# Kernel tuning notes

Measured on AMD Instinct MI355X. Metric: run time of the kernel, lower is better.

The kernel has to match this reference:

```python
import jax, jax.numpy as jnp
import numpy as np

B, LQ, LKV = 4, 2048, 2048
E, AUG, H = 2048, 1024, 16
DH = E // H
EPS = 1e-6


def setup_inputs() -> dict:
    key = jax.random.key(0)
    ks = jax.random.split(key, 6)
    s = lambda d: 1.0 / np.sqrt(d)
    return {
        "query": jax.random.normal(ks[0], (B, LQ, E), jnp.float32),
        "aug_hidden_state": jax.random.normal(ks[1], (B, LKV, AUG), jnp.float32),
        "aug_mask": jnp.ones((B, LKV), jnp.float32),
        "proj_w": jax.random.normal(ks[2], (E, AUG), jnp.float32) * s(AUG),
        "proj_b": jnp.zeros((E,), jnp.float32),
        "in_proj_w": jax.random.normal(ks[3], (3 * E, E), jnp.float32) * s(E),
        "in_proj_b": jnp.zeros((3 * E,), jnp.float32),
        "out_proj_w": jax.random.normal(ks[4], (E, E), jnp.float32) * s(E),
        "out_proj_b": jnp.zeros((E,), jnp.float32),
        "rms_w": jnp.zeros((E,), jnp.float32),
    }


def reference(query, aug_hidden_state, aug_mask, proj_w, proj_b,
              in_proj_w, in_proj_b, out_proj_w, out_proj_b, rms_w):
    del aug_mask  # asserted but never used by the original forward
    # key and value: two identical Linear calls in the original -> same tensor
    kv = aug_hidden_state @ proj_w.T + proj_b                      # [B,LKV,E]
    wq, wk, wv = jnp.split(in_proj_w, 3, axis=0)
    bq, bk, bv = jnp.split(in_proj_b, 3, axis=0)
    q = (query @ wq.T + bq).reshape(B, LQ, H, DH)
    k = (kv @ wk.T + bk).reshape(B, LKV, H, DH)
    v = (kv @ wv.T + bv).reshape(B, LKV, H, DH)
    scale = 1.0 / np.sqrt(DH)
    scores = jnp.einsum("bqhd,bkhd->bhqk", q * scale, k)           # [B,H,LQ,LKV]
    attn = jax.nn.softmax(scores, axis=-1)
    ctx = jnp.einsum("bhqk,bkhd->bqhd", attn, v).reshape(B, LQ, E)
    attn_out = ctx @ out_proj_w.T + out_proj_b                      # [B,LQ,E]
    # GemmaRMSNorm: fp32 norm, (1 + weight) gain
    x32 = attn_out.astype(jnp.float32)
    normed = x32 * jax.lax.rsqrt(jnp.mean(x32 * x32, axis=-1, keepdims=True) + EPS)
    attn_out = (normed * (1.0 + rms_w)).astype(attn_out.dtype)
    return attn_out + query
```

## Files before the change

kernel.cpp:

```cpp
#include <hip/hip_runtime.h>
#include <hip/hip_bf16.h>
#include <stdint.h>

#define B_   4
#define LQ_  2048
#define LKV_ 2048
#define E_   2048
#define AUG_ 1024
#define H_   16
#define DH_  128

typedef unsigned short u16;
typedef __bf16 bf16x8 __attribute__((ext_vector_type(8)));
typedef float f32x4 __attribute__((ext_vector_type(4)));
typedef float f32x16 __attribute__((ext_vector_type(16)));
typedef int i32x2 __attribute__((ext_vector_type(2)));

__device__ __forceinline__ u16 f2bf(float f) {
  union { float f; unsigned u; } v; v.f = f;
  unsigned r = v.u + 0x7fffu + ((v.u >> 16) & 1u);
  return (u16)(r >> 16);
}
__device__ __forceinline__ unsigned pk2(float a, float b) {
  return (unsigned)f2bf(a) | ((unsigned)f2bf(b) << 16);
}
__device__ __forceinline__ float bf2f(u16 u) {
  union { unsigned u; float f; } v; v.u = (unsigned)u << 16; return v.f;
}
__device__ __forceinline__ unsigned cvtpk_bf16(float lo, float hi) {
  unsigned r;
  asm("v_cvt_pk_bf16_f32 %0, %1, %2" : "=v"(r) : "v"(lo), "v"(hi));
  return r;
}
__device__ __forceinline__ float fast_ex2(float x) {
  float r;
  asm("v_exp_f32 %0, %1" : "=v"(r) : "v"(x));
  return r;
}

#define GLDS(gsrc, ldst)                                                        \
  __builtin_amdgcn_global_load_lds(                                             \
      (__attribute__((address_space(1))) void*)(uintptr_t)(gsrc),               \
      (__attribute__((address_space(3))) void*)(unsigned)(uintptr_t)(ldst),     \
      16, 0, 0)

#define BARRIER()                                   \
  do {                                              \
    asm volatile("" ::: "memory");                  \
    __builtin_amdgcn_s_barrier();                   \
    asm volatile("" ::: "memory");                  \
  } while (0)

__global__ __launch_bounds__(256) void cast5(const float* __restrict__ p0, u16* __restrict__ o0, int c0,
                                             const float* __restrict__ p1, u16* __restrict__ o1, int c1,
                                             const float* __restrict__ p2, u16* __restrict__ o2, int c2,
                                             const float* __restrict__ p3, u16* __restrict__ o3, int c3,
                                             const float* __restrict__ p4, u16* __restrict__ o4, int c4) {
  int stride = gridDim.x * blockDim.x;
  for (int i = blockIdx.x * blockDim.x + threadIdx.x; i < c4; i += stride) {
    const float* in; u16* out; int j;
    if (i < c0)      { in = p0; out = o0; j = i; }
    else if (i < c1) { in = p1; out = o1; j = i - c0; }
    else if (i < c2) { in = p2; out = o2; j = i - c1; }
    else if (i < c3) { in = p3; out = o3; j = i - c2; }
    else             { in = p4; out = o4; j = i - c3; }
    const float4* p = (const float4*)in + (size_t)j * 2;
    float4 a = p[0], b = p[1];
    uint4 o;
    o.x = pk2(a.x, a.y); o.y = pk2(a.z, a.w);
    o.z = pk2(b.x, b.y); o.w = pk2(b.z, b.w);
    ((uint4*)out)[j] = o;
  }
}

template <int OUTF32>
__global__ __launch_bounds__(512, 2) void gemm_bt2(const u16* __restrict__ A,
                                                   const u16* __restrict__ W,
                                                   const float* __restrict__ bias,
                                                   void* __restrict__ Cp,
                                                   int N, int K) {
  __shared__ __align__(16) u16 As[3][256 * 32];
  __shared__ __align__(16) u16 Bs[3][256 * 32];
  const int tid = threadIdx.x;
  const int wave = tid >> 6, lane = tid & 63;
  const int wr = wave >> 2, wc = wave & 3;
  const int g = lane >> 4, r16 = lane & 15;
  const int m0 = blockIdx.y << 8, n0 = blockIdx.x << 8;

  size_t gA[2], gB[2];
  int ldst[2];
#pragma unroll
  for (int i = 0; i < 2; ++i) {
    int c = tid + i * 512;
    int s = c >> 6, w = c & 63;
    int wp = w ^ (((w >> 5) & 1) << 1);
    int grow = s * 16 + (wp >> 2);
    int gcol = (wp & 3) * 8;
    gA[i] = (size_t)(m0 + grow) * K + gcol;
    gB[i] = (size_t)(n0 + grow) * K + gcol;
    ldst[i] = c * 8;
  }
  const int aoff = r16 * 32 + ((g * 8) ^ ((r16 & 8) ? 16 : 0));

  f32x4 acc[8][4];
#pragma unroll
  for (int m = 0; m < 8; ++m)
#pragma unroll
    for (int n = 0; n < 4; ++n) acc[m][n] = (f32x4){0.f, 0.f, 0.f, 0.f};

  const int NT = K >> 5;
#pragma unroll
  for (int i = 0; i < 2; ++i) GLDS(A + gA[i], &As[0][ldst[i]]);
#pragma unroll
  for (int i = 0; i < 2; ++i) GLDS(W + gB[i], &Bs[0][ldst[i]]);
#pragma unroll
  for (int i = 0; i < 2; ++i) GLDS(A + gA[i] + 32, &As[1][ldst[i]]);
#pragma unroll
  for (int i = 0; i < 2; ++i) GLDS(W + gB[i] + 32, &Bs[1][ldst[i]]);

  int cur = 0;
  for (int t = 0; t < NT; ++t) {
    if (t + 1 < NT)
      asm volatile("s_waitcnt vmcnt(4)" ::: "memory");
    else
      asm volatile("s_waitcnt vmcnt(0)" ::: "memory");
    BARRIER();

    const u16* as = As[cur];
    const u16* bs = Bs[cur];
    int nxt = cur + 2; if (nxt >= 3) nxt -= 3;

    bf16x8 bfr[4], af[4];
#pragma unroll
    for (int n = 0; n < 4; ++n)
      bfr[n] = *(const bf16x8*)&bs[wc * 2048 + n * 512 + aoff];
#pragma unroll
    for (int m = 0; m < 4; ++m)
      af[m] = *(const bf16x8*)&as[wr * 4096 + m * 512 + aoff];
    if (t + 2 < NT) {
      size_t k0 = (size_t)(t + 2) * 32;
#pragma unroll
      for (int i = 0; i < 2; ++i) GLDS(A + gA[i] + k0, &As[nxt][ldst[i]]);
    }
    __builtin_amdgcn_s_setprio(1);
#pragma unroll
    for (int m = 0; m < 4; ++m)
#pragma unroll
      for (int n = 0; n < 4; ++n)
        acc[m][n] = __builtin_amdgcn_mfma_f32_16x16x32_bf16(af[m], bfr[n], acc[m][n], 0, 0, 0);
    __builtin_amdgcn_s_setprio(0);

    bf16x8 af2[4];
#pragma unroll
    for (int m = 0; m < 4; ++m)
      af2[m] = *(const bf16x8*)&as[wr * 4096 + (m + 4) * 512 + aoff];
    if (t + 2 < NT) {
      size_t k0 = (size_t)(t + 2) * 32;
#pragma unroll
      for (int i = 0; i < 2; ++i) GLDS(W + gB[i] + k0, &Bs[nxt][ldst[i]]);
    }
    __builtin_amdgcn_s_setprio(1);
#pragma unroll
    for (int m = 0; m < 4; ++m)
#pragma unroll
      for (int n = 0; n < 4; ++n)
        acc[m + 4][n] = __builtin_amdgcn_mfma_f32_16x16x32_bf16(af2[m], bfr[n], acc[m + 4][n], 0, 0, 0);
    __builtin_amdgcn_s_setprio(0);

    cur = cur + 1; if (cur >= 3) cur -= 3;
  }

  float bv[4];
#pragma unroll
  for (int n = 0; n < 4; ++n)
    bv[n] = bias ? bias[n0 + wc * 64 + n * 16 + r16] : 0.f;
#pragma unroll
  for (int m = 0; m < 8; ++m) {
    int row = m0 + wr * 128 + m * 16 + g * 4;
#pragma unroll
    for (int n = 0; n < 4; ++n) {
      int col = n0 + wc * 64 + n * 16 + r16;
#pragma unroll
      for (int r = 0; r < 4; ++r) {
        float v = acc[m][n][r] + bv[n];
        if (OUTF32)
          ((float*)Cp)[(size_t)(row + r) * N + col] = v;
        else
          ((u16*)Cp)[(size_t)(row + r) * N + col] = f2bf(v);
      }
    }
  }
}

__global__ __launch_bounds__(256) void transpose_v(const u16* __restrict__ v,
                                                   u16* __restrict__ vt) {
  __shared__ __align__(16) u16 t[64][72];
  int tid = threadIdx.x;
  int bh = blockIdx.z, b = bh >> 4, h = bh & 15;
  int kv0 = blockIdx.x << 6, d0 = blockIdx.y << 6;
  int gr = tid & 7, rw = tid >> 3;
#pragma unroll
  for (int p = 0; p < 2; ++p) {
    int row = rw + p * 32;
    uint4 x = *(const uint4*)&v[((size_t)(b * LKV_) + kv0 + row) * E_ + h * DH_ + d0 + gr * 8];
    *(uint4*)&t[row][gr * 8] = x;
  }
  __syncthreads();
#pragma unroll
  for (int p = 0; p < 2; ++p) {
    int d = rw + p * 32;
    u16 tmp[8];
#pragma unroll
    for (int j = 0; j < 8; ++j) tmp[j] = t[gr * 8 + j][d];
    uint4 o;
    o.x = (unsigned)tmp[0] | ((unsigned)tmp[1] << 16);
    o.y = (unsigned)tmp[2] | ((unsigned)tmp[3] << 16);
    o.z = (unsigned)tmp[4] | ((unsigned)tmp[5] << 16);
    o.w = (unsigned)tmp[6] | ((unsigned)tmp[7] << 16);
    *(uint4*)&vt[(((size_t)(b * H_ + h)) * DH_ + d0 + d) * LKV_ + kv0 + gr * 8] = o;
  }
}

__global__ __launch_bounds__(256) void attn_kernel(const u16* __restrict__ Q,
                                                   const u16* __restrict__ K,
                                                   const u16* __restrict__ Vt,
                                                   u16* __restrict__ Octx) {
  __shared__ __align__(16) u16 Ks[2][64 * 128];
  __shared__ __align__(16) u16 Vs[2][128 * 64];
  const int tid = threadIdx.x, wave = tid >> 6, lane = tid & 63;
  const int bid = blockIdx.x;
  const int qb = bid & 15, bh = bid >> 4, b = bh >> 4, h = bh & 15;
  const int q0 = qb << 7;
  const int l31 = lane & 31, hi = lane >> 5;
  const float Cs = 0.08838834764831845f * 1.4426950408889634f;

  const u16* Qp = Q + ((size_t)(b * LQ_ + q0 + wave * 32 + l31)) * E_ + h * DH_;
  const u16* Kp = K + ((size_t)(b * LKV_)) * E_ + h * DH_;
  const u16* Vp = Vt + (size_t)bh * DH_ * LKV_;

  const int kl_row = lane >> 4, kl_g = lane & 15;
  const int vl_row = lane >> 3, vl_g = lane & 7;

  bf16x8 qf[8];
#pragma unroll
  for (int c = 0; c < 8; ++c) {
    bf16x8 raw = *(const bf16x8*)&Qp[c * 16 + hi * 8];
#pragma unroll
    for (int j = 0; j < 8; ++j) qf[c][j] = (__bf16)((float)raw[j] * Cs);
  }

  bf16x8 VONES;
#pragma unroll
  for (int j = 0; j < 8; ++j) VONES[j] = (__bf16)1.0f;
  f32x16 FZERO = {};

  f32x16 o[4];
#pragma unroll
  for (int d = 0; d < 4; ++d)
#pragma unroll
    for (int r = 0; r < 16; ++r) o[d][r] = 0.f;
  f32x16 ol = {};

  auto STAGE = [&](int kv0, int buf) {
#pragma unroll
    for (int j = 0; j < 4; ++j) {
      int cc = wave * 4 + j;
      int krow = cc * 4 + kl_row;
      GLDS(Kp + (size_t)(kv0 + krow) * E_ + ((kl_g ^ (krow & 15)) << 3), &Ks[buf][cc * 512]);
      int vrow = cc * 8 + vl_row;
      GLDS(Vp + (size_t)vrow * LKV_ + kv0 + ((vl_g ^ (vrow & 7)) << 3), &Vs[buf][cc * 512]);
    }
  };

  const int NT = LKV_ / 64;
  STAGE(0, 0);

  for (int t = 0; t < NT; ++t) {
    const int cur = t & 1;
    if (t + 1 < NT) {
      STAGE((t + 1) * 64, cur ^ 1);
      asm volatile("s_waitcnt vmcnt(8)" ::: "memory");
    } else {
      asm volatile("s_waitcnt vmcnt(0)" ::: "memory");
    }
    BARRIER();

    const u16* ks = Ks[cur];
    const u16* vs = Vs[cur];

    f32x16 st[2];
#pragma unroll
    for (int n = 0; n < 2; ++n) {
      int row = n * 32 + l31;
      bf16x8 kf = *(const bf16x8*)&ks[row * 128 + ((hi ^ (row & 15)) << 3)];
      st[n] = __builtin_amdgcn_mfma_f32_32x32x16_bf16(kf, qf[0], FZERO, 0, 0, 0);
    }
#pragma unroll
    for (int c = 1; c < 8; ++c) {
#pragma unroll
      for (int n = 0; n < 2; ++n) {
        int row = n * 32 + l31;
        bf16x8 kf = *(const bf16x8*)&ks[row * 128 + (((c * 2 + hi) ^ (row & 15)) << 3)];
        st[n] = __builtin_amdgcn_mfma_f32_32x32x16_bf16(kf, qf[c], st[n], 0, 0, 0);
      }
    }

    unsigned AF[4][4];
#pragma unroll
    for (int n = 0; n < 2; ++n) {
      float pv[16];
#pragma unroll
      for (int r = 0; r < 16; ++r) pv[r] = fast_ex2(st[n][r]);
      unsigned a0 = cvtpk_bf16(pv[0], pv[1]),   a1 = cvtpk_bf16(pv[2], pv[3]);
      unsigned a2 = cvtpk_bf16(pv[4], pv[5]),   a3 = cvtpk_bf16(pv[6], pv[7]);
      unsigned b0 = cvtpk_bf16(pv[8], pv[9]),   b1 = cvtpk_bf16(pv[10], pv[11]);
      unsigned b2 = cvtpk_bf16(pv[12], pv[13]), b3 = cvtpk_bf16(pv[14], pv[15]);
      i32x2 r02 = __builtin_amdgcn_permlane32_swap((int)a0, (int)a2, false, false);
      i32x2 r13 = __builtin_amdgcn_permlane32_swap((int)a1, (int)a3, false, false);
      AF[n * 2][0] = (unsigned)r02[0]; AF[n * 2][1] = (unsigned)r13[0];
      AF[n * 2][2] = (unsigned)r02[1]; AF[n * 2][3] = (unsigned)r13[1];
      i32x2 s02 = __builtin_amdgcn_permlane32_swap((int)b0, (int)b2, false, false);
      i32x2 s13 = __builtin_amdgcn_permlane32_swap((int)b1, (int)b3, false, false);
      AF[n * 2 + 1][0] = (unsigned)s02[0]; AF[n * 2 + 1][1] = (unsigned)s13[0];
      AF[n * 2 + 1][2] = (unsigned)s02[1]; AF[n * 2 + 1][3] = (unsigned)s13[1];
    }

#pragma unroll
    for (int s = 0; s < 4; ++s) {
      union { unsigned u[4]; bf16x8 v; } pk;
      pk.u[0] = AF[s][0]; pk.u[1] = AF[s][1]; pk.u[2] = AF[s][2]; pk.u[3] = AF[s][3];
      bf16x8 pa = pk.v;
#pragma unroll
      for (int db = 0; db < 4; ++db) {
        int d = db * 32 + l31;
        bf16x8 vf = *(const bf16x8*)&vs[d * 64 + (((s * 2 + hi) ^ (d & 7)) << 3)];
        o[db] = __builtin_amdgcn_mfma_f32_32x32x16_bf16(pa, vf, o[db], 0, 0, 0);
      }
      ol = __builtin_amdgcn_mfma_f32_32x32x16_bf16(pa, VONES, ol, 0, 0, 0);
    }
    BARRIER();
  }

#pragma unroll
  for (int r = 0; r < 16; ++r) {
    int crow = (r & 3) + 8 * (r >> 2) + 4 * hi;
    float li = 1.0f / ol[r];
    size_t rb = ((size_t)(b * LQ_ + q0 + wave * 32 + crow)) * E_ + h * DH_ + l31;
#pragma unroll
    for (int db = 0; db < 4; ++db)
      Octx[rb + db * 32] = f2bf(o[db][r] * li);
  }
}

__global__ __launch_bounds__(256) void rms_res_bf(const u16* __restrict__ x,
                                                  const float* __restrict__ w,
                                                  const float* __restrict__ qres,
                                                  float* __restrict__ out) {
  int row = blockIdx.x, tid = threadIdx.x;
  uint4 xv = ((const uint4*)(x + (size_t)row * E_))[tid];
  float xf[8];
  xf[0] = bf2f((u16)(xv.x & 0xffff)); xf[1] = bf2f((u16)(xv.x >> 16));
  xf[2] = bf2f((u16)(xv.y & 0xffff)); xf[3] = bf2f((u16)(xv.y >> 16));
  xf[4] = bf2f((u16)(xv.z & 0xffff)); xf[5] = bf2f((u16)(xv.z >> 16));
  xf[6] = bf2f((u16)(xv.w & 0xffff)); xf[7] = bf2f((u16)(xv.w >> 16));
  float ss = 0.f;
#pragma unroll
  for (int j = 0; j < 8; ++j) ss += xf[j] * xf[j];
  ss += __shfl_xor(ss, 1);  ss += __shfl_xor(ss, 2);
  ss += __shfl_xor(ss, 4);  ss += __shfl_xor(ss, 8);
  ss += __shfl_xor(ss, 16); ss += __shfl_xor(ss, 32);
  __shared__ float ls[4];
  if ((tid & 63) == 0) ls[tid >> 6] = ss;
  __syncthreads();
  float total = ls[0] + ls[1] + ls[2] + ls[3];
  float rs = rsqrtf(total * (1.0f / (float)E_) + 1e-6f);
  const float4* qr = (const float4*)(qres + (size_t)row * E_);
  const float4* wr4 = (const float4*)w;
  float4 q0 = qr[tid * 2], q1 = qr[tid * 2 + 1];
  float4 w0 = wr4[tid * 2], w1 = wr4[tid * 2 + 1];
  float4 o0, o1;
  o0.x = xf[0] * rs * (1.f + w0.x) + q0.x;
  o0.y = xf[1] * rs * (1.f + w0.y) + q0.y;
  o0.z = xf[2] * rs * (1.f + w0.z) + q0.z;
  o0.w = xf[3] * rs * (1.f + w0.w) + q0.w;
  o1.x = xf[4] * rs * (1.f + w1.x) + q1.x;
  o1.y = xf[5] * rs * (1.f + w1.y) + q1.y;
  o1.z = xf[6] * rs * (1.f + w1.z) + q1.z;
  o1.w = xf[7] * rs * (1.f + w1.w) + q1.w;
  float4* op = (float4*)(out + (size_t)row * E_);
  op[tid * 2] = o0;
  op[tid * 2 + 1] = o1;
}

extern "C" void kernel_launch(void* const* d_in, const int* in_sizes, int n_in,
                              void* d_out, int out_size, void* d_ws, size_t ws_size,
                              hipStream_t stream) {
  const float* query = (const float*)d_in[0];
  const float* aug   = (const float*)d_in[1];
  const float* projw = (const float*)d_in[3];
  const float* projb = (const float*)d_in[4];
  const float* ipw   = (const float*)d_in[5];
  const float* ipb   = (const float*)d_in[6];
  const float* opw   = (const float*)d_in[7];
  const float* opb   = (const float*)d_in[8];
  const float* rmsw  = (const float*)d_in[9];

  char* ws = (char*)d_ws;
  size_t off = 0;
  auto alloc = [&](size_t bytes) {
    void* p = ws + off;
    off += (bytes + 1023) & ~(size_t)1023;
    return p;
  };
  u16* query_bf = (u16*)alloc((size_t)B_ * LQ_ * E_ * 2);
  u16* aug_bf   = (u16*)alloc((size_t)B_ * LKV_ * AUG_ * 2);
  u16* projw_bf = (u16*)alloc((size_t)E_ * AUG_ * 2);
  u16* w_bf     = (u16*)alloc((size_t)3 * E_ * E_ * 2);
  u16* outw_bf  = (u16*)alloc((size_t)E_ * E_ * 2);
  u16* kv_bf    = (u16*)alloc((size_t)B_ * LKV_ * E_ * 2);
  u16* q_bf     = (u16*)alloc((size_t)B_ * LQ_ * E_ * 2);
  u16* k_bf     = (u16*)alloc((size_t)B_ * LKV_ * E_ * 2);
  u16* v_bf     = (u16*)alloc((size_t)B_ * LKV_ * E_ * 2);
  u16* ctx_bf   = (u16*)alloc((size_t)B_ * LQ_ * E_ * 2);
  u16* attn_out = query_bf;
  u16* vt_bf = kv_bf;
  (void)in_sizes; (void)n_in; (void)ws_size;

  const int M = B_ * LQ_;

  const int n8_q  = (int)((size_t)M * E_ / 8);
  const int n8_a  = (int)((size_t)M * AUG_ / 8);
  const int n8_pw = (int)((size_t)E_ * AUG_ / 8);
  const int n8_iw = (int)((size_t)3 * E_ * E_ / 8);
  const int n8_ow = (int)((size_t)E_ * E_ / 8);
  const int cc0 = n8_q, cc1 = cc0 + n8_a, cc2 = cc1 + n8_pw, cc3 = cc2 + n8_iw,
            cc4 = cc3 + n8_ow;
  cast5<<<2048, 256, 0, stream>>>(query, query_bf, cc0,
                                  aug, aug_bf, cc1,
                                  projw, projw_bf, cc2,
                                  ipw, w_bf, cc3,
                                  opw, outw_bf, cc4);

  gemm_bt2<0><<<dim3(E_ / 256, M / 256), 512, 0, stream>>>(aug_bf, projw_bf, projb, kv_bf, E_, AUG_);
  gemm_bt2<0><<<dim3(E_ / 256, M / 256), 512, 0, stream>>>(query_bf, w_bf, ipb, q_bf, E_, E_);
  gemm_bt2<0><<<dim3(E_ / 256, M / 256), 512, 0, stream>>>(kv_bf, w_bf + (size_t)E_ * E_, ipb + E_, k_bf, E_, E_);
  gemm_bt2<0><<<dim3(E_ / 256, M / 256), 512, 0, stream>>>(kv_bf, w_bf + (size_t)2 * E_ * E_, ipb + 2 * E_, v_bf, E_, E_);
  transpose_v<<<dim3(LKV_ / 64, DH_ / 64, B_ * H_), 256, 0, stream>>>(v_bf, vt_bf);
  attn_kernel<<<B_ * H_ * (LQ_ / 128), 256, 0, stream>>>(q_bf, k_bf, vt_bf, ctx_bf);
  gemm_bt2<0><<<dim3(E_ / 256, M / 256), 512, 0, stream>>>(ctx_bf, outw_bf, opb, attn_out, E_, E_);
  rms_res_bf<<<M, 256, 0, stream>>>(attn_out, rmsw, query, (float*)d_out);
}
```

Measured before the change: 524.2 us.

## Fold KV projection into K/V in-projection weights to skip intermediate GEMM

Precomputes the fused weights Wk·Wproj and Wv·Wproj (plus fused biases through a small GEMV), then computes K and V directly from the augmented hidden state with K=1024 instead of running a separate kv projection and two K=2048 GEMMs. This cuts activation-side GEMM FLOPs substantially in exchange for a small weight-weight GEMM and a transpose each call. The fused weights are rounded to bf16 once more, which adds a little numerical error.

Result: faster. 477.1 us (-9.0%).

```diff
diff --git a/kernel.cpp b/kernel.cpp
--- a/kernel.cpp
+++ b/kernel.cpp
@@ -190,6 +190,56 @@
       }
     }
   }
+}
+
+__global__ __launch_bounds__(256) void transpose_w(const u16* __restrict__ in,
+                                                   u16* __restrict__ out,
+                                                   int R, int C) {
+  __shared__ __align__(16) u16 t[64][72];
+  int tid = threadIdx.x;
+  int c0 = blockIdx.x << 6, r0 = blockIdx.y << 6;
+  int gr = tid & 7, rw = tid >> 3;
+#pragma unroll
+  for (int p = 0; p < 2; ++p) {
+    int row = rw + p * 32;
+    uint4 x = *(const uint4*)&in[(size_t)(r0 + row) * C + c0 + gr * 8];
+    *(uint4*)&t[row][gr * 8] = x;
+  }
+  __syncthreads();
+#pragma unroll
+  for (int p = 0; p < 2; ++p) {
+    int d = rw + p * 32;
+    u16 tmp[8];
+#pragma unroll
+    for (int j = 0; j < 8; ++j) tmp[j] = t[gr * 8 + j][d];
+    uint4 o;
+    o.x = (unsigned)tmp[0] | ((unsigned)tmp[1] << 16);
+    o.y = (unsigned)tmp[2] | ((unsigned)tmp[3] << 16);
+    o.z = (unsigned)tmp[4] | ((unsigned)tmp[5] << 16);
+    o.w = (unsigned)tmp[6] | ((unsigned)tmp[7] << 16);
+    *(uint4*)&out[(size_t)(c0 + d) * R + r0 + gr * 8] = o;
+  }
+}
+
+__global__ __launch_bounds__(256) void gemv_bias(const u16* __restrict__ W,
+                                                 const float* __restrict__ pb,
+                                                 const float* __restrict__ base,
+                                                 float* __restrict__ out, int K) {
+  int row = blockIdx.x, tid = threadIdx.x;
+  uint4 wv = ((const uint4*)(W + (size_t)row * K))[tid];
+  const float4* pb4 = (const float4*)pb;
+  float4 p0 = pb4[tid * 2], p1 = pb4[tid * 2 + 1];
+  float s = bf2f((u16)(wv.x & 0xffff)) * p0.x + bf2f((u16)(wv.x >> 16)) * p0.y +
+            bf2f((u16)(wv.y & 0xffff)) * p0.z + bf2f((u16)(wv.y >> 16)) * p0.w +
+            bf2f((u16)(wv.z & 0xffff)) * p1.x + bf2f((u16)(wv.z >> 16)) * p1.y +
+            bf2f((u16)(wv.w & 0xffff)) * p1.z + bf2f((u16)(wv.w >> 16)) * p1.w;
+  s += __shfl_xor(s, 1);  s += __shfl_xor(s, 2);
+  s += __shfl_xor(s, 4);  s += __shfl_xor(s, 8);
+  s += __shfl_xor(s, 16); s += __shfl_xor(s, 32);
+  __shared__ float ls[4];
+  if ((tid & 63) == 0) ls[tid >> 6] = s;
+  __syncthreads();
+  if (tid == 0) out[row] = ls[0] + ls[1] + ls[2] + ls[3] + base[row];
 }
 
 __global__ __launch_bounds__(256) void transpose_v(const u16* __restrict__ v,
@@ -423,6 +473,9 @@
   u16* v_bf     = (u16*)alloc((size_t)B_ * LKV_ * E_ * 2);
   u16* ctx_bf   = (u16*)alloc((size_t)B_ * LQ_ * E_ * 2);
   u16* attn_out = query_bf;
+  u16* projwT = kv_bf;
+  u16* wkv_f  = kv_bf + (size_t)AUG_ * E_;
+  float* bkv  = (float*)(kv_bf + (size_t)AUG_ * E_ + (size_t)2 * E_ * AUG_);
   u16* vt_bf = kv_bf;
   (void)in_sizes; (void)n_in; (void)ws_size;
 
@@ -441,10 +494,15 @@
                                   ipw, w_bf, cc3,
                                   opw, outw_bf, cc4);
 
-  gemm_bt2<0><<<dim3(E_ / 256, M / 256), 512, 0, stream>>>(aug_bf, projw_bf, projb, kv_bf, E_, AUG_);
+  transpose_w<<<dim3(AUG_ / 64, E_ / 64), 256, 0, stream>>>(projw_bf, projwT, E_, AUG_);
+  gemm_bt2<0><<<dim3(AUG_ / 256, (2 * E_) / 256), 512, 0, stream>>>(
+      w_bf + (size_t)E_ * E_, projwT, nullptr, wkv_f, AUG_, E_);
+  gemv_bias<<<2 * E_, 256, 0, stream>>>(w_bf + (size_t)E_ * E_, projb, ipb + E_, bkv, E_);
+
   gemm_bt2<0><<<dim3(E_ / 256, M / 256), 512, 0, stream>>>(query_bf, w_bf, ipb, q_bf, E_, E_);
-  gemm_bt2<0><<<dim3(E_ / 256, M / 256), 512, 0, stream>>>(kv_bf, w_bf + (size_t)E_ * E_, ipb + E_, k_bf, E_, E_);
-  gemm_bt2<0><<<dim3(E_ / 256, M / 256), 512, 0, stream>>>(kv_bf, w_bf + (size_t)2 * E_ * E_, ipb + 2 * E_, v_bf, E_, E_);
+  gemm_bt2<0><<<dim3(E_ / 256, M / 256), 512, 0, stream>>>(aug_bf, wkv_f, bkv, k_bf, E_, AUG_);
+  gemm_bt2<0><<<dim3(E_ / 256, M / 256), 512, 0, stream>>>(
+      aug_bf, wkv_f + (size_t)E_ * AUG_, bkv + E_, v_bf, E_, AUG_);
   transpose_v<<<dim3(LKV_ / 64, DH_ / 64, B_ * H_), 256, 0, stream>>>(v_bf, vt_bf);
   attn_kernel<<<B_ * H_ * (LQ_ / 128), 256, 0, stream>>>(q_bf, k_bf, vt_bf, ctx_bf);
   gemm_bt2<0><<<dim3(E_ / 256, M / 256), 512, 0, stream>>>(ctx_bf, outw_bf, opb, attn_out, E_, E_);
```
